# Kernel optimization log

Measured on AMD Instinct MI355X. Metric: run time of the kernel, lower is better.

## Reference

```python
import jax, jax.numpy as jnp
import numpy as np

V, D, B, S = 32000, 1024, 4, 2048
EPS = 1e-12  # matches torch F.normalize eps


def setup_inputs() -> dict:
    key = jax.random.key(0)
    k1, k2, k3 = jax.random.split(key, 3)
    init_embed = jax.random.normal(k1, (V, D), dtype=jnp.float32)
    scale = np.sqrt(D).astype(np.float32)  # default scale = sqrt(embed_dim)
    norm = jnp.maximum(jnp.linalg.norm(init_embed, axis=-1, keepdims=True), EPS)
    in_weight = scale * (init_embed / norm)            # [V, D]
    out_weight = init_embed.T                          # [D, V]
    inputs = jax.random.randint(k2, (B, S), 0, V)      # token ids
    embeds = jax.random.normal(k3, (B, S, D), dtype=jnp.float32)
    return {"inputs": inputs, "embeds": embeds, "in_weight": in_weight, "out_weight": out_weight}


def reference(inputs, embeds, in_weight, out_weight):
    # embed(): one_hot @ in_weight is mathematically an index gather
    embedded = jnp.take(in_weight, inputs, axis=0)          # [B, S, D]
    # unembed(): dense matmul against transposed embedding table
    logits = jnp.einsum('bsd,dv->bsv', embeds, out_weight)  # [B, S, V]
    return embedded, logits
```

## Files before the change

### kernel.cpp

```cpp
#include <hip/hip_runtime.h>
#include <hip/hip_bf16.h>
#include <stdint.h>

#define V_SZ 32000
#define D_SZ 1024
#define M_SZ 8192

typedef __attribute__((ext_vector_type(8))) short bf16x8;
typedef __attribute__((ext_vector_type(4))) float f32x4;
typedef __attribute__((ext_vector_type(16))) float f32x16;

static __device__ __forceinline__ unsigned short f32_to_bf16_rne(float f) {
    union { float f; uint32_t u; } v; v.f = f;
    uint32_t u = v.u;
    uint32_t lsb = (u >> 16) & 1;
    u += 0x7fffu + lsb;
    return (unsigned short)(u >> 16);
}

__global__ void gather_rows(const int* __restrict__ ids,
                            const float* __restrict__ table,
                            float* __restrict__ out) {
    int row = blockIdx.x;
    int id  = ids[row];
    const f32x4* src = (const f32x4*)(table + (size_t)id * D_SZ);
    f32x4*       dst = (f32x4*)(out + (size_t)row * D_SZ);
    __builtin_nontemporal_store(src[threadIdx.x], &dst[threadIdx.x]);
}

__global__ void cast_f32_bf16(const float* __restrict__ in,
                              unsigned short* __restrict__ out, int n8) {
    int i = blockIdx.x * blockDim.x + threadIdx.x;
    int stride = gridDim.x * blockDim.x;
    for (; i < n8; i += stride) {
        const float4* p = (const float4*)(in + (size_t)i * 8);
        float4 a = p[0], b = p[1];
        union { unsigned short s[8]; uint4 v; } r;
        r.s[0] = f32_to_bf16_rne(a.x); r.s[1] = f32_to_bf16_rne(a.y);
        r.s[2] = f32_to_bf16_rne(a.z); r.s[3] = f32_to_bf16_rne(a.w);
        r.s[4] = f32_to_bf16_rne(b.x); r.s[5] = f32_to_bf16_rne(b.y);
        r.s[6] = f32_to_bf16_rne(b.z); r.s[7] = f32_to_bf16_rne(b.w);
        ((uint4*)out)[i] = r.v;
    }
}

__global__ void transpose_cast(const float* __restrict__ w,
                               unsigned short* __restrict__ bt) {
    __shared__ unsigned short tile[32][34];
    int n0 = blockIdx.x * 32;
    int k0 = blockIdx.y * 32;
    int r = threadIdx.x >> 5;
    int c = threadIdx.x & 31;
#pragma unroll
    for (int rr = 0; rr < 32; rr += 8) {
        float v = w[(size_t)(k0 + r + rr) * V_SZ + (n0 + c)];
        tile[c][r + rr] = f32_to_bf16_rne(v);
    }
    __syncthreads();
    int nl = threadIdx.x >> 3;
    int ks = threadIdx.x & 7;
    union { unsigned short s[4]; uint2 v; } r2;
#pragma unroll
    for (int j = 0; j < 4; ++j) r2.s[j] = tile[nl][ks * 4 + j];
    ((uint2*)(bt + (size_t)(n0 + nl) * D_SZ + k0))[ks] = r2.v;
}

#define BM 256
#define BN 256
#define BK 64
#define NT (D_SZ / BK)

static __device__ __forceinline__ void gload_lds16(const unsigned short* g, void* lds) {
    __builtin_amdgcn_global_load_lds(
        (const __attribute__((address_space(1))) void*)g,
        (__attribute__((address_space(3))) void*)lds,
        16, 0, 0);
}

__global__ __launch_bounds__(512, 2)
void gemm_bf16_8p(const unsigned short* __restrict__ A,
                  const unsigned short* __restrict__ Bt,
                  float* __restrict__ C) {
    __shared__ __align__(16) char lds[131072];

    const int tid  = threadIdx.x;
    const int lane = tid & 63;
    const int w    = tid >> 6;
    const int wr   = w >> 2;
    const int wc   = w & 3;

    const int bid = blockIdx.x;
    const int xcd = bid & 7;
    const int j   = bid >> 3;
    const int bm0 = (xcd * 4 + (j & 3)) * BM;
    const int bn0 = (j >> 2) * BN;

    const int hi0  = tid >> 7;
    const int row0 = tid & 127;
    const int dstO = hi0 * 2048 + row0 * 16;
    const unsigned short* gA = A  + (size_t)(bm0 + row0) * D_SZ + hi0 * 8;
    const unsigned short* gB = Bt + (size_t)(bn0 + row0) * D_SZ + hi0 * 8;

#define STG(ptr, slotbase) do { \
    gload_lds16((ptr),      (char*)lds + (slotbase) + dstO); \
    gload_lds16((ptr) + 32, (char*)lds + (slotbase) + dstO + 8192); } while (0)

    STG(gB,                           32768);
    STG(gB + (size_t)128 * D_SZ,      32768 + 16384);
    STG(gA,                           0);
    STG(gA + (size_t)128 * D_SZ,      16384);
    STG(gB + 64,                      65536 + 32768);
    STG(gB + (size_t)128 * D_SZ + 64, 65536 + 32768 + 16384);
    STG(gA + 64,                      65536);
    asm volatile("s_waitcnt vmcnt(6)" ::: "memory");
    __builtin_amdgcn_s_barrier();

    const unsigned short* pA1 = gA + (size_t)128 * D_SZ + 64;
    const unsigned short* pB0 = gB + 128;
    const unsigned short* pB1 = gB + (size_t)128 * D_SZ + 128;
    const unsigned short* pA0 = gA + 128;

    f32x16 acc[4][2];
#pragma unroll
    for (int m = 0; m < 4; ++m)
#pragma unroll
        for (int n = 0; n < 2; ++n)
#pragma unroll
            for (int e = 0; e < 16; ++e) acc[m][n][e] = 0.0f;

    bf16x8 a[2][4];
    bf16x8 b[2][4];

    const int base_f = (lane >> 5) * 2048 + (lane & 31) * 16;

#define LDA(mi2, kk, QM) (*(const bf16x8*)(abuf + (kk) * 4096 + ((QM) * 2 + (mi2)) * 512 + base_f))
#define LDB(ni, kk)      (*(const bf16x8*)(bbuf + (kk) * 4096 + (ni) * 512 + base_f))

#define MFMA_Q(QM, QN) \
    __builtin_amdgcn_s_setprio(1); \
    _Pragma("unroll") for (int kk = 0; kk < 4; ++kk) \
    _Pragma("unroll") for (int mi2 = 0; mi2 < 2; ++mi2) \
        acc[(QM) * 2 + mi2][QN] = __builtin_amdgcn_mfma_f32_32x32x16_bf16( \
            a[mi2][kk], b[QN][kk], acc[(QM) * 2 + mi2][QN], 0, 0, 0); \
    __builtin_amdgcn_s_setprio(0);

#define MIDSYNC \
    __builtin_amdgcn_sched_barrier(0); \
    __builtin_amdgcn_s_barrier();

    for (int t = 0; t < NT; ++t) {
        const int   dbuf = (t & 1) << 16;
        const char* abuf = (const char*)lds + dbuf + wr * 16384;
        const char* bbuf = (const char*)lds + dbuf + 32768
                           + (wc >> 1) * 16384 + (wc & 1) * 1024;
        const int nslot = (dbuf ^ 65536);

        a[0][0] = LDA(0, 0, 0); a[0][1] = LDA(0, 1, 0);
        a[0][2] = LDA(0, 2, 0); a[0][3] = LDA(0, 3, 0);
        a[1][0] = LDA(1, 0, 0); a[1][1] = LDA(1, 1, 0);
        a[1][2] = LDA(1, 2, 0); a[1][3] = LDA(1, 3, 0);
        b[0][0] = LDB(0, 0); b[0][1] = LDB(0, 1);
        b[0][2] = LDB(0, 2); b[0][3] = LDB(0, 3);
        if (t + 1 < NT) STG(pA1, nslot + 16384);
        MIDSYNC;
        MFMA_Q(0, 0);
        __builtin_amdgcn_s_barrier();

        b[1][0] = LDB(1, 0); b[1][1] = LDB(1, 1);
        b[1][2] = LDB(1, 2); b[1][3] = LDB(1, 3);
        MIDSYNC;
        MFMA_Q(0, 1);
        __builtin_amdgcn_s_barrier();

        a[0][0] = LDA(0, 0, 1); a[0][1] = LDA(0, 1, 1);
        a[0][2] = LDA(0, 2, 1); a[0][3] = LDA(0, 3, 1);
        a[1][0] = LDA(1, 0, 1); a[1][1] = LDA(1, 1, 1);
        a[1][2] = LDA(1, 2, 1); a[1][3] = LDA(1, 3, 1);
        if (t + 2 < NT) STG(pB0, dbuf + 32768);
        MIDSYNC;
        MFMA_Q(1, 1);
        __builtin_amdgcn_s_barrier();

        if (t + 2 < NT) { STG(pB1, dbuf + 32768 + 16384); STG(pA0, dbuf); }
        MFMA_Q(1, 0);
        if (t < NT - 2)       { asm volatile("s_waitcnt vmcnt(6)" ::: "memory"); }
        else if (t == NT - 2) { asm volatile("s_waitcnt vmcnt(0)" ::: "memory"); }
        __builtin_amdgcn_s_barrier();

        pA1 += BK; pB0 += BK; pB1 += BK; pA0 += BK;
    }

    const int crow = bm0 + wr * 128 + (lane >> 5) * 4;
    const int ccol = bn0 + wc * 64 + (lane & 31);
#pragma unroll
    for (int mi = 0; mi < 4; ++mi)
#pragma unroll
        for (int ni = 0; ni < 2; ++ni) {
            float* base = C + (size_t)(crow + mi * 32) * V_SZ + (ccol + ni * 32);
#pragma unroll
            for (int r = 0; r < 16; ++r) {
                int roff = (r & 3) + 8 * (r >> 2);
                __builtin_nontemporal_store(acc[mi][ni][r], base + (size_t)roff * V_SZ);
            }
        }
#undef STG
#undef LDA
#undef LDB
#undef MFMA_Q
#undef MIDSYNC
}

extern "C" void kernel_launch(void* const* d_in, const int* in_sizes, int n_in,
                              void* d_out, int out_size, void* d_ws, size_t ws_size,
                              hipStream_t stream) {
    const int*   ids        = (const int*)d_in[0];
    const float* embeds     = (const float*)d_in[1];
    const float* in_weight  = (const float*)d_in[2];
    const float* out_weight = (const float*)d_in[3];

    float* out_embedded = (float*)d_out;
    float* out_logits   = (float*)d_out + (size_t)M_SZ * D_SZ;

    unsigned short* Abf  = (unsigned short*)d_ws;
    unsigned short* Btbf = Abf + (size_t)M_SZ * D_SZ;

    gather_rows<<<M_SZ, 256, 0, stream>>>(ids, in_weight, out_embedded);
    cast_f32_bf16<<<2048, 256, 0, stream>>>(embeds, Abf, M_SZ * D_SZ / 8);
    transpose_cast<<<dim3(V_SZ / 32, D_SZ / 32), 256, 0, stream>>>(out_weight, Btbf);
    gemm_bf16_8p<<<dim3((V_SZ / BN) * (M_SZ / BM)), 512, 0, stream>>>(Abf, Btbf, out_logits);
}
```

Baseline: 759.8 us.

## Shrink GEMM tile to 128x128 with 4-wave blocks and simpler pipeline

Replaces the 256x256-tile, 8-wave GEMM with a 128x128-tile, 4-wave kernel using 64 KB of double-buffered LDS and a two-phase load/MFMA schedule per K step. The block-to-XCD mapping is adjusted so each XCD covers 8 M-tiles. Smaller tiles give more blocks and less LDS per block, which may improve occupancy and tail balance. In exchange, each tile has lower arithmetic intensity and global/L2 traffic for A and B roughly doubles.

```diff
diff --git a/kernel.cpp b/kernel.cpp
--- a/kernel.cpp
+++ b/kernel.cpp
@@ -65,8 +65,8 @@
     ((uint2*)(bt + (size_t)(n0 + nl) * D_SZ + k0))[ks] = r2.v;
 }
 
-#define BM 256
-#define BN 256
+#define BM 128
+#define BN 128
 #define BK 64
 #define NT (D_SZ / BK)
 
@@ -77,23 +77,23 @@
         16, 0, 0);
 }
 
-__global__ __launch_bounds__(512, 2)
-void gemm_bf16_8p(const unsigned short* __restrict__ A,
+__global__ __launch_bounds__(256, 2)
+void gemm_bf16_2b(const unsigned short* __restrict__ A,
                   const unsigned short* __restrict__ Bt,
                   float* __restrict__ C) {
-    __shared__ __align__(16) char lds[131072];
+    __shared__ __align__(16) char lds[65536];
 
     const int tid  = threadIdx.x;
     const int lane = tid & 63;
     const int w    = tid >> 6;
-    const int wr   = w >> 2;
-    const int wc   = w & 3;
+    const int wr   = w >> 1;
+    const int wc   = w & 1;
 
     const int bid = blockIdx.x;
     const int xcd = bid & 7;
     const int j   = bid >> 3;
-    const int bm0 = (xcd * 4 + (j & 3)) * BM;
-    const int bn0 = (j >> 2) * BN;
+    const int bm0 = (xcd * 8 + (j & 7)) * BM;
+    const int bn0 = (j >> 3) * BN;
 
     const int hi0  = tid >> 7;
     const int row0 = tid & 127;
@@ -101,113 +101,82 @@
     const unsigned short* gA = A  + (size_t)(bm0 + row0) * D_SZ + hi0 * 8;
     const unsigned short* gB = Bt + (size_t)(bn0 + row0) * D_SZ + hi0 * 8;
 
-#define STG(ptr, slotbase) do { \
-    gload_lds16((ptr),      (char*)lds + (slotbase) + dstO); \
-    gload_lds16((ptr) + 32, (char*)lds + (slotbase) + dstO + 8192); } while (0)
-
-    STG(gB,                           32768);
-    STG(gB + (size_t)128 * D_SZ,      32768 + 16384);
-    STG(gA,                           0);
-    STG(gA + (size_t)128 * D_SZ,      16384);
-    STG(gB + 64,                      65536 + 32768);
-    STG(gB + (size_t)128 * D_SZ + 64, 65536 + 32768 + 16384);
-    STG(gA + 64,                      65536);
-    asm volatile("s_waitcnt vmcnt(6)" ::: "memory");
+#define STG_A(tt, db) { _Pragma("unroll") for (int k_ = 0; k_ < 4; ++k_) \
+    gload_lds16(gA + (tt) * 64 + k_ * 16, (char*)lds + (db) + dstO + k_ * 4096); }
+#define STG_B(tt, db) { _Pragma("unroll") for (int k_ = 0; k_ < 4; ++k_) \
+    gload_lds16(gB + (tt) * 64 + k_ * 16, (char*)lds + (db) + 16384 + dstO + k_ * 4096); }
+
+    STG_A(0, 0); STG_B(0, 0); STG_A(1, 32768);
+    asm volatile("s_waitcnt vmcnt(4)" ::: "memory");
     __builtin_amdgcn_s_barrier();
 
-    const unsigned short* pA1 = gA + (size_t)128 * D_SZ + 64;
-    const unsigned short* pB0 = gB + 128;
-    const unsigned short* pB1 = gB + (size_t)128 * D_SZ + 128;
-    const unsigned short* pA0 = gA + 128;
-
-    f32x16 acc[4][2];
-#pragma unroll
-    for (int m = 0; m < 4; ++m)
+    f32x16 acc[2][2];
+#pragma unroll
+    for (int g = 0; g < 2; ++g)
 #pragma unroll
         for (int n = 0; n < 2; ++n)
 #pragma unroll
-            for (int e = 0; e < 16; ++e) acc[m][n][e] = 0.0f;
+            for (int e = 0; e < 16; ++e) acc[g][n][e] = 0.0f;
 
     bf16x8 a[2][4];
-    bf16x8 b[2][4];
+    bf16x8 b[4];
 
     const int base_f = (lane >> 5) * 2048 + (lane & 31) * 16;
 
-#define LDA(mi2, kk, QM) (*(const bf16x8*)(abuf + (kk) * 4096 + ((QM) * 2 + (mi2)) * 512 + base_f))
-#define LDB(ni, kk)      (*(const bf16x8*)(bbuf + (kk) * 4096 + (ni) * 512 + base_f))
-
-#define MFMA_Q(QM, QN) \
+#define LDA(g, kk) (*(const bf16x8*)(abuf + (kk) * 4096 + (g) * 512 + base_f))
+#define LDB(n, kk) (*(const bf16x8*)(bbuf + (kk) * 4096 + (n) * 512 + base_f))
+
+#define MFMA_N(N) \
     __builtin_amdgcn_s_setprio(1); \
     _Pragma("unroll") for (int kk = 0; kk < 4; ++kk) \
-    _Pragma("unroll") for (int mi2 = 0; mi2 < 2; ++mi2) \
-        acc[(QM) * 2 + mi2][QN] = __builtin_amdgcn_mfma_f32_32x32x16_bf16( \
-            a[mi2][kk], b[QN][kk], acc[(QM) * 2 + mi2][QN], 0, 0, 0); \
+    _Pragma("unroll") for (int g = 0; g < 2; ++g) \
+        acc[g][N] = __builtin_amdgcn_mfma_f32_32x32x16_bf16( \
+            a[g][kk], b[kk], acc[g][N], 0, 0, 0); \
     __builtin_amdgcn_s_setprio(0);
 
-#define MIDSYNC \
-    __builtin_amdgcn_sched_barrier(0); \
-    __builtin_amdgcn_s_barrier();
-
     for (int t = 0; t < NT; ++t) {
-        const int   dbuf = (t & 1) << 16;
-        const char* abuf = (const char*)lds + dbuf + wr * 16384;
-        const char* bbuf = (const char*)lds + dbuf + 32768
-                           + (wc >> 1) * 16384 + (wc & 1) * 1024;
-        const int nslot = (dbuf ^ 65536);
-
-        a[0][0] = LDA(0, 0, 0); a[0][1] = LDA(0, 1, 0);
-        a[0][2] = LDA(0, 2, 0); a[0][3] = LDA(0, 3, 0);
-        a[1][0] = LDA(1, 0, 0); a[1][1] = LDA(1, 1, 0);
-        a[1][2] = LDA(1, 2, 0); a[1][3] = LDA(1, 3, 0);
-        b[0][0] = LDB(0, 0); b[0][1] = LDB(0, 1);
-        b[0][2] = LDB(0, 2); b[0][3] = LDB(0, 3);
-        if (t + 1 < NT) STG(pA1, nslot + 16384);
-        MIDSYNC;
-        MFMA_Q(0, 0);
-        __builtin_amdgcn_s_barrier();
-
-        b[1][0] = LDB(1, 0); b[1][1] = LDB(1, 1);
-        b[1][2] = LDB(1, 2); b[1][3] = LDB(1, 3);
-        MIDSYNC;
-        MFMA_Q(0, 1);
-        __builtin_amdgcn_s_barrier();
-
-        a[0][0] = LDA(0, 0, 1); a[0][1] = LDA(0, 1, 1);
-        a[0][2] = LDA(0, 2, 1); a[0][3] = LDA(0, 3, 1);
-        a[1][0] = LDA(1, 0, 1); a[1][1] = LDA(1, 1, 1);
-        a[1][2] = LDA(1, 2, 1); a[1][3] = LDA(1, 3, 1);
-        if (t + 2 < NT) STG(pB0, dbuf + 32768);
-        MIDSYNC;
-        MFMA_Q(1, 1);
-        __builtin_amdgcn_s_barrier();
-
-        if (t + 2 < NT) { STG(pB1, dbuf + 32768 + 16384); STG(pA0, dbuf); }
-        MFMA_Q(1, 0);
-        if (t < NT - 2)       { asm volatile("s_waitcnt vmcnt(6)" ::: "memory"); }
+        const int   dbuf  = (t & 1) * 32768;
+        const int   ndbuf = dbuf ^ 32768;
+        const char* abuf  = (const char*)lds + dbuf + wr * 1024;
+        const char* bbuf  = (const char*)lds + dbuf + 16384 + wc * 1024;
+
+        a[0][0] = LDA(0, 0); a[0][1] = LDA(0, 1); a[0][2] = LDA(0, 2); a[0][3] = LDA(0, 3);
+        a[1][0] = LDA(1, 0); a[1][1] = LDA(1, 1); a[1][2] = LDA(1, 2); a[1][3] = LDA(1, 3);
+        b[0] = LDB(0, 0); b[1] = LDB(0, 1); b[2] = LDB(0, 2); b[3] = LDB(0, 3);
+        if (t + 1 < NT) STG_B(t + 1, ndbuf);
+        __builtin_amdgcn_sched_barrier(0);
+        __builtin_amdgcn_s_barrier();
+        MFMA_N(0);
+        __builtin_amdgcn_s_barrier();
+
+        b[0] = LDB(1, 0); b[1] = LDB(1, 1); b[2] = LDB(1, 2); b[3] = LDB(1, 3);
+        if (t + 2 < NT) STG_A(t + 2, dbuf);
+        __builtin_amdgcn_sched_barrier(0);
+        __builtin_amdgcn_s_barrier();
+        MFMA_N(1);
+        if (t < NT - 2)       { asm volatile("s_waitcnt vmcnt(4)" ::: "memory"); }
         else if (t == NT - 2) { asm volatile("s_waitcnt vmcnt(0)" ::: "memory"); }
         __builtin_amdgcn_s_barrier();
-
-        pA1 += BK; pB0 += BK; pB1 += BK; pA0 += BK;
     }
 
-    const int crow = bm0 + wr * 128 + (lane >> 5) * 4;
+    const int crow = bm0 + wr * 64 + (lane >> 5) * 4;
     const int ccol = bn0 + wc * 64 + (lane & 31);
 #pragma unroll
-    for (int mi = 0; mi < 4; ++mi)
-#pragma unroll
-        for (int ni = 0; ni < 2; ++ni) {
-            float* base = C + (size_t)(crow + mi * 32) * V_SZ + (ccol + ni * 32);
+    for (int g = 0; g < 2; ++g)
+#pragma unroll
+        for (int n = 0; n < 2; ++n) {
+            float* base = C + (size_t)(crow + g * 32) * V_SZ + (ccol + n * 32);
 #pragma unroll
             for (int r = 0; r < 16; ++r) {
                 int roff = (r & 3) + 8 * (r >> 2);
-                __builtin_nontemporal_store(acc[mi][ni][r], base + (size_t)roff * V_SZ);
+                __builtin_nontemporal_store(acc[g][n][r], base + (size_t)roff * V_SZ);
             }
         }
-#undef STG
+#undef STG_A
+#undef STG_B
 #undef LDA
 #undef LDB
-#undef MFMA_Q
-#undef MIDSYNC
+#undef MFMA_N
 }
 
 extern "C" void kernel_launch(void* const* d_in, const int* in_sizes, int n_in,
@@ -227,5 +196,5 @@
     gather_rows<<<M_SZ, 256, 0, stream>>>(ids, in_weight, out_embedded);
     cast_f32_bf16<<<2048, 256, 0, stream>>>(embeds, Abf, M_SZ * D_SZ / 8);
     transpose_cast<<<dim3(V_SZ / 32, D_SZ / 32), 256, 0, stream>>>(out_weight, Btbf);
-    gemm_bf16_8p<<<dim3((V_SZ / BN) * (M_SZ / BM)), 512, 0, stream>>>(Abf, Btbf, out_logits);
-}
+    gemm_bf16_2b<<<dim3((V_SZ / BN) * (M_SZ / BM)), 256, 0, stream>>>(Abf, Btbf, out_logits);
+}
```

After: 1.007 ms. +32.5%, slower.

## Make GEMM persistent with 256 blocks streaming N tiles and cross-tile prefetch

Applied to the files above, without the earlier changes.

The GEMM launch changes from 4000 one-tile blocks to 256 persistent blocks. Each block keeps a fixed M row-block and walks 15 or 16 N tiles with a stride of 8 tiles. The last K steps of each tile prefetch the first B slices of the next tile, so the load pipeline stays full across tile boundaries and launch/prologue overhead per tile goes away. The cost is that the epilogue stores are serialized inside each block, not overlapped by other blocks. Load is also unbalanced, since some blocks get 16 tiles and others 15, and the A panel is reloaded for each tile.

```diff
diff --git a/kernel.cpp b/kernel.cpp
--- a/kernel.cpp
+++ b/kernel.cpp
@@ -68,7 +68,7 @@
 #define BM 256
 #define BN 256
 #define BK 64
-#define NT (D_SZ / BK)
+#define NSTEP (D_SZ / BK)
 
 static __device__ __forceinline__ void gload_lds16(const unsigned short* g, void* lds) {
     __builtin_amdgcn_global_load_lds(
@@ -78,7 +78,7 @@
 }
 
 __global__ __launch_bounds__(512, 2)
-void gemm_bf16_8p(const unsigned short* __restrict__ A,
+void gemm_persist(const unsigned short* __restrict__ A,
                   const unsigned short* __restrict__ Bt,
                   float* __restrict__ C) {
     __shared__ __align__(16) char lds[131072];
@@ -91,34 +91,32 @@
 
     const int bid = blockIdx.x;
     const int xcd = bid & 7;
-    const int j   = bid >> 3;
-    const int bm0 = (xcd * 4 + (j & 3)) * BM;
-    const int bn0 = (j >> 2) * BN;
+    const int jb  = bid >> 3;
+    const int bm0 = (xcd * 4 + (jb & 3)) * BM;
+    const int q0  = jb >> 2;
+    const int ntiles = (bid < 160) ? 16 : 15;
 
     const int hi0  = tid >> 7;
     const int row0 = tid & 127;
     const int dstO = hi0 * 2048 + row0 * 16;
     const unsigned short* gA = A  + (size_t)(bm0 + row0) * D_SZ + hi0 * 8;
-    const unsigned short* gB = Bt + (size_t)(bn0 + row0) * D_SZ + hi0 * 8;
+    const unsigned short* gA1 = gA + (size_t)128 * D_SZ;
+    const unsigned short* gBc = Bt + (size_t)(q0 * BN + row0) * D_SZ + hi0 * 8;
+    const size_t bn_stride = (size_t)8 * BN * D_SZ;
 
 #define STG(ptr, slotbase) do { \
     gload_lds16((ptr),      (char*)lds + (slotbase) + dstO); \
     gload_lds16((ptr) + 32, (char*)lds + (slotbase) + dstO + 8192); } while (0)
 
-    STG(gB,                           32768);
-    STG(gB + (size_t)128 * D_SZ,      32768 + 16384);
-    STG(gA,                           0);
-    STG(gA + (size_t)128 * D_SZ,      16384);
-    STG(gB + 64,                      65536 + 32768);
-    STG(gB + (size_t)128 * D_SZ + 64, 65536 + 32768 + 16384);
-    STG(gA + 64,                      65536);
+    STG(gBc,                           32768);
+    STG(gBc + (size_t)128 * D_SZ,      32768 + 16384);
+    STG(gA,                            0);
+    STG(gA1,                           16384);
+    STG(gBc + 64,                      65536 + 32768);
+    STG(gBc + (size_t)128 * D_SZ + 64, 65536 + 32768 + 16384);
+    STG(gA + 64,                       65536);
     asm volatile("s_waitcnt vmcnt(6)" ::: "memory");
     __builtin_amdgcn_s_barrier();
-
-    const unsigned short* pA1 = gA + (size_t)128 * D_SZ + 64;
-    const unsigned short* pB0 = gB + 128;
-    const unsigned short* pB1 = gB + (size_t)128 * D_SZ + 128;
-    const unsigned short* pA0 = gA + 128;
 
     f32x16 acc[4][2];
 #pragma unroll
@@ -148,61 +146,83 @@
     __builtin_amdgcn_sched_barrier(0); \
     __builtin_amdgcn_s_barrier();
 
-    for (int t = 0; t < NT; ++t) {
-        const int   dbuf = (t & 1) << 16;
-        const char* abuf = (const char*)lds + dbuf + wr * 16384;
-        const char* bbuf = (const char*)lds + dbuf + 32768
-                           + (wc >> 1) * 16384 + (wc & 1) * 1024;
-        const int nslot = (dbuf ^ 65536);
-
-        a[0][0] = LDA(0, 0, 0); a[0][1] = LDA(0, 1, 0);
-        a[0][2] = LDA(0, 2, 0); a[0][3] = LDA(0, 3, 0);
-        a[1][0] = LDA(1, 0, 0); a[1][1] = LDA(1, 1, 0);
-        a[1][2] = LDA(1, 2, 0); a[1][3] = LDA(1, 3, 0);
-        b[0][0] = LDB(0, 0); b[0][1] = LDB(0, 1);
-        b[0][2] = LDB(0, 2); b[0][3] = LDB(0, 3);
-        if (t + 1 < NT) STG(pA1, nslot + 16384);
-        MIDSYNC;
-        MFMA_Q(0, 0);
-        __builtin_amdgcn_s_barrier();
-
-        b[1][0] = LDB(1, 0); b[1][1] = LDB(1, 1);
-        b[1][2] = LDB(1, 2); b[1][3] = LDB(1, 3);
-        MIDSYNC;
-        MFMA_Q(0, 1);
-        __builtin_amdgcn_s_barrier();
-
-        a[0][0] = LDA(0, 0, 1); a[0][1] = LDA(0, 1, 1);
-        a[0][2] = LDA(0, 2, 1); a[0][3] = LDA(0, 3, 1);
-        a[1][0] = LDA(1, 0, 1); a[1][1] = LDA(1, 1, 1);
-        a[1][2] = LDA(1, 2, 1); a[1][3] = LDA(1, 3, 1);
-        if (t + 2 < NT) STG(pB0, dbuf + 32768);
-        MIDSYNC;
-        MFMA_Q(1, 1);
-        __builtin_amdgcn_s_barrier();
-
-        if (t + 2 < NT) { STG(pB1, dbuf + 32768 + 16384); STG(pA0, dbuf); }
-        MFMA_Q(1, 0);
-        if (t < NT - 2)       { asm volatile("s_waitcnt vmcnt(6)" ::: "memory"); }
-        else if (t == NT - 2) { asm volatile("s_waitcnt vmcnt(0)" ::: "memory"); }
-        __builtin_amdgcn_s_barrier();
-
-        pA1 += BK; pB0 += BK; pB1 += BK; pA0 += BK;
+    const int crow = bm0 + wr * 128 + (lane >> 5) * 4;
+    const int ccol_f = wc * 64 + (lane & 31);
+
+    for (int r = 0; r < ntiles; ++r) {
+        const unsigned short* gBn = gBc + bn_stride;
+        const bool last = (r == ntiles - 1);
+
+        for (int t = 0; t < NSTEP; ++t) {
+            const int   dbuf = (t & 1) << 16;
+            const char* abuf = (const char*)lds + dbuf + wr * 16384;
+            const char* bbuf = (const char*)lds + dbuf + 32768
+                               + (wc >> 1) * 16384 + (wc & 1) * 1024;
+            const int nslot = (dbuf ^ 65536);
+
+            a[0][0] = LDA(0, 0, 0); a[0][1] = LDA(0, 1, 0);
+            a[0][2] = LDA(0, 2, 0); a[0][3] = LDA(0, 3, 0);
+            a[1][0] = LDA(1, 0, 0); a[1][1] = LDA(1, 1, 0);
+            a[1][2] = LDA(1, 2, 0); a[1][3] = LDA(1, 3, 0);
+            b[0][0] = LDB(0, 0); b[0][1] = LDB(0, 1);
+            b[0][2] = LDB(0, 2); b[0][3] = LDB(0, 3);
+            if (!(last && t == 15)) STG(gA1 + ((t + 1) & 15) * 64, nslot + 16384);
+            MIDSYNC;
+            MFMA_Q(0, 0);
+            __builtin_amdgcn_s_barrier();
+
+            b[1][0] = LDB(1, 0); b[1][1] = LDB(1, 1);
+            b[1][2] = LDB(1, 2); b[1][3] = LDB(1, 3);
+            MIDSYNC;
+            MFMA_Q(0, 1);
+            __builtin_amdgcn_s_barrier();
+
+            a[0][0] = LDA(0, 0, 1); a[0][1] = LDA(0, 1, 1);
+            a[0][2] = LDA(0, 2, 1); a[0][3] = LDA(0, 3, 1);
+            a[1][0] = LDA(1, 0, 1); a[1][1] = LDA(1, 1, 1);
+            a[1][2] = LDA(1, 2, 1); a[1][3] = LDA(1, 3, 1);
+            if (t < 14 || !last) {
+                const unsigned short* pb = (t < 14) ? gBc + (t + 2) * 64
+                                                    : gBn + (t - 14) * 64;
+                STG(pb, dbuf + 32768);
+            }
+            MIDSYNC;
+            MFMA_Q(1, 1);
+            __builtin_amdgcn_s_barrier();
+
+            if (t < 14 || !last) {
+                const unsigned short* pb = (t < 14) ? gBc + (t + 2) * 64
+                                                    : gBn + (t - 14) * 64;
+                STG(pb + (size_t)128 * D_SZ, dbuf + 32768 + 16384);
+                STG(gA + ((t + 2) & 15) * 64, dbuf);
+            }
+            MFMA_Q(1, 0);
+            if (last && t >= 14) { asm volatile("s_waitcnt vmcnt(0)" ::: "memory"); }
+            else                 { asm volatile("s_waitcnt vmcnt(6)" ::: "memory"); }
+            __builtin_amdgcn_s_barrier();
+        }
+
+        const int ccol = (q0 + 8 * r) * BN + ccol_f;
+#pragma unroll
+        for (int mi = 0; mi < 4; ++mi)
+#pragma unroll
+            for (int ni = 0; ni < 2; ++ni) {
+                float* base = C + (size_t)(crow + mi * 32) * V_SZ + (ccol + ni * 32);
+#pragma unroll
+                for (int e = 0; e < 16; ++e) {
+                    int roff = (e & 3) + 8 * (e >> 2);
+                    __builtin_nontemporal_store(acc[mi][ni][e], base + (size_t)roff * V_SZ);
+                }
+            }
+#pragma unroll
+        for (int m = 0; m < 4; ++m)
+#pragma unroll
+            for (int n = 0; n < 2; ++n)
+#pragma unroll
+                for (int e = 0; e < 16; ++e) acc[m][n][e] = 0.0f;
+
+        gBc = gBn;
     }
-
-    const int crow = bm0 + wr * 128 + (lane >> 5) * 4;
-    const int ccol = bn0 + wc * 64 + (lane & 31);
-#pragma unroll
-    for (int mi = 0; mi < 4; ++mi)
-#pragma unroll
-        for (int ni = 0; ni < 2; ++ni) {
-            float* base = C + (size_t)(crow + mi * 32) * V_SZ + (ccol + ni * 32);
-#pragma unroll
-            for (int r = 0; r < 16; ++r) {
-                int roff = (r & 3) + 8 * (r >> 2);
-                __builtin_nontemporal_store(acc[mi][ni][r], base + (size_t)roff * V_SZ);
-            }
-        }
 #undef STG
 #undef LDA
 #undef LDB
@@ -227,5 +247,5 @@
     gather_rows<<<M_SZ, 256, 0, stream>>>(ids, in_weight, out_embedded);
     cast_f32_bf16<<<2048, 256, 0, stream>>>(embeds, Abf, M_SZ * D_SZ / 8);
     transpose_cast<<<dim3(V_SZ / 32, D_SZ / 32), 256, 0, stream>>>(out_weight, Btbf);
-    gemm_bf16_8p<<<dim3((V_SZ / BN) * (M_SZ / BM)), 512, 0, stream>>>(Abf, Btbf, out_logits);
-}
+    gemm_persist<<<dim3(256), 512, 0, stream>>>(Abf, Btbf, out_logits);
+}
```

After: 676.7 us. -10.9%, faster.
